# Performance work log

Measured on AMD Instinct MI355X. Metric: run time of the kernel, lower is better.

## Reference

```python
import jax, jax.numpy as jnp
import numpy as np

THRESH = 0.5     # confidence threshold (forward arg 'thresh' in the original)
IOU_THR = 0.1    # nms(boxes, 0.1) in the original
K = 512          # fixed top-k candidates per scale (static-shape stand-in for nonzero())


def _decode(output, anchors, stride, k):
    """Filter + parse for one scale. output: [B, 3*(5+nc), H, W]."""
    B, C, H, W = output.shape
    o = output.transpose(0, 2, 3, 1).reshape(B, H, W, 3, -1)   # [B,H,W,3,5+nc]
    D = o.shape[-1]
    conf = jax.nn.sigmoid(o[..., 0]).reshape(-1)               # [B*H*W*3]
    scores, idx = jax.lax.top_k(conf, k)                       # fixed-size filter
    n, h, w, a = jnp.unravel_index(idx, (B, H, W, 3))
    v = o.reshape(-1, D)[idx]                                  # [K, 5+nc]
    dt = v.dtype
    cy = (h.astype(dt) + jax.nn.sigmoid(v[:, 2])) * stride
    cx = (w.astype(dt) + jax.nn.sigmoid(v[:, 1])) * stride
    bw = anchors[a, 0] * jnp.exp(v[:, 3])
    bh = anchors[a, 1] * jnp.exp(v[:, 4])
    cond = jax.nn.sigmoid(v[:, 0])
    cls = jnp.argmax(v[:, 5:], axis=1).astype(dt)              # argmax(softmax)=argmax
    boxes = jnp.stack([n.astype(dt), cond, cx, cy, bw, bh, cls], axis=1)  # [K,7]
    valid = cond > THRESH
    return boxes, valid


def _nms(boxes, valid, iou_thr):
    """Greedy per-image, per-class NMS. boxes: [N,7] = (n, cond, cx, cy, w, h, cls)."""
    N = boxes.shape[0]
    score = jnp.where(valid, boxes[:, 1], -jnp.inf)
    order = jnp.argsort(-score)
    b = boxes[order]
    val = valid[order]
    x1 = b[:, 2] - b[:, 4] * 0.5
    y1 = b[:, 3] - b[:, 5] * 0.5
    x2 = b[:, 2] + b[:, 4] * 0.5
    y2 = b[:, 3] + b[:, 5] * 0.5
    area = b[:, 4] * b[:, 5]
    ix1 = jnp.maximum(x1[:, None], x1[None, :])
    iy1 = jnp.maximum(y1[:, None], y1[None, :])
    ix2 = jnp.minimum(x2[:, None], x2[None, :])
    iy2 = jnp.minimum(y2[:, None], y2[None, :])
    inter = jnp.clip(ix2 - ix1, 0) * jnp.clip(iy2 - iy1, 0)
    iou = inter / (area[:, None] + area[None, :] - inter + 1e-9)
    same = (b[:, 0, None] == b[None, :, 0]) & (b[:, 6, None] == b[None, :, 6])
    overlap = (iou > iou_thr) & same                           # [N,N] bool, no grad needed
    rng = jnp.arange(N)

    def body(i, supp):
        row = overlap[i] & (rng > i)
        active = (~supp[i]) & val[i]
        return jnp.where(active, supp | row, supp)

    supp = jax.lax.fori_loop(0, N, body, jnp.zeros(N, bool))
    keep = val & (~supp)
    return b * keep[:, None].astype(b.dtype), keep


def setup_inputs() -> dict:
    key = jax.random.key(0)
    ks = jax.random.split(key, 6)
    B, C = 64, 255  # 3 * (5 + 80 classes)
    return {
        "output_13": jax.random.normal(ks[0], (B, C, 13, 13), jnp.float32),
        "output_26": jax.random.normal(ks[1], (B, C, 26, 26), jnp.float32),
        "output_52": jax.random.normal(ks[2], (B, C, 52, 52), jnp.float32),
        "anchors_13": jax.random.uniform(ks[3], (3, 2), jnp.float32, 90.0, 330.0),
        "anchors_26": jax.random.uniform(ks[4], (3, 2), jnp.float32, 30.0, 120.0),
        "anchors_52": jax.random.uniform(ks[5], (3, 2), jnp.float32, 10.0, 60.0),
    }


def reference(output_13, output_26, output_52, anchors_13, anchors_26, anchors_52):
    b13, v13 = _decode(output_13, anchors_13, 32.0, K)
    b26, v26 = _decode(output_26, anchors_26, 16.0, K)
    b52, v52 = _decode(output_52, anchors_52, 8.0, K)
    boxes = jnp.concatenate([b13, b26, b52], axis=0)   # [3K, 7]
    valid = jnp.concatenate([v13, v26, v52], axis=0)
    final_boxes, keep = _nms(boxes, valid, IOU_THR)
    return final_boxes, keep
```

## Files before the change

### kernel.cpp

```cpp
#include <hip/hip_runtime.h>
#include <stdint.h>

#define K_SEL 512
#define NBOX 1536
#define CAND_CAP 4096
#define HBITS 13
#define HBINS 8192
#define NSHARD 128
#define SEG 128
#define HBLK 64
#define HB0 8
#define HB1 16
#define HB2 40
#define ICAP 56

#define M0 32448
#define M1 129792
#define M2 519168
#define M_TOT (M0+M1+M2)

#define OFF_HIST 0u
#define OFF_CNT  98304u
#define OFF_THR  99840u
#define OFF_CAND 99872u
#define OFF_BOX  493088u
#define OFF_SKEY 536096u
#define OFF_TOPK 548384u
#define ZERO_BYTES 99840u

typedef unsigned long long u64;
typedef uint32_t u32;
typedef uint16_t u16;

__device__ __forceinline__ float sigf(float x) { return 1.0f / (1.0f + expf(-x)); }

__device__ __forceinline__ u32 fmono(float f) {
    u32 u = __float_as_uint(f);
    return (u & 0x80000000u) ? ~u : (u | 0x80000000u);
}

__global__ __launch_bounds__(1024) void k_hist(const float* p0, const float* p1, const float* p2,
                                               uint8_t* ws) {
    __shared__ u32 lh[HBINS];
    for (int i = threadIdx.x; i < HBINS; i += 1024) lh[i] = 0;
    __syncthreads();
    int b = blockIdx.x, s, b0, nb;
    if (b < HB0)            { s = 0; b0 = b;             nb = HB0; }
    else if (b < HB0 + HB1) { s = 1; b0 = b - HB0;       nb = HB1; }
    else                    { s = 2; b0 = b - HB0 - HB1; nb = HB2; }
    int M = (s == 0) ? M0 : (s == 1) ? M1 : M2;
    int H = (s == 0) ? 13 : (s == 1) ? 26 : 52;
    int HW = H * H;
    const float* p = (s == 0) ? p0 : (s == 1) ? p1 : p2;
    for (int o = b0 * 1024 + threadIdx.x; o < M; o += nb * 1024) {
        int n = o / (3 * HW); int rem = o - n * 3 * HW;
        int a = rem / HW;     int pix = rem - a * HW;
        float conf = sigf(p[(size_t)(n * 255 + a * 85) * HW + pix]);
        atomicAdd(&lh[fmono(conf) >> (32 - HBITS)], 1u);
    }
    __syncthreads();
    u32* gh = (u32*)(ws + OFF_HIST) + s * HBINS;
    for (int i = threadIdx.x; i < HBINS; i += 1024) {
        u32 v = lh[i];
        if (v) atomicAdd(&gh[i], v);
    }
}

__global__ __launch_bounds__(1024) void k_scan(uint8_t* ws) {
    int s = blockIdx.x;
    u32* hist = (u32*)(ws + OFF_HIST) + s * HBINS;
    __shared__ u32 sum[1024];
    int t = threadIdx.x;
    u32 bins[8];
    const uint4* hp = (const uint4*)(hist + t * 8);
    uint4 x = hp[0], y = hp[1];
    bins[0] = x.x; bins[1] = x.y; bins[2] = x.z; bins[3] = x.w;
    bins[4] = y.x; bins[5] = y.y; bins[6] = y.z; bins[7] = y.w;
    u32 acc = 0;
#pragma unroll
    for (int k = 0; k < 8; ++k) acc += bins[k];
    sum[t] = acc;
    __syncthreads();
    for (int off = 1; off < 1024; off <<= 1) {
        u32 v = (t + off < 1024) ? sum[t + off] : 0;
        __syncthreads();
        sum[t] += v;
        __syncthreads();
    }
    u32 excl = (t < 1023) ? sum[t + 1] : 0;
    u32 mine = sum[t] - excl;
    if (excl < K_SEL && excl + mine >= K_SEL) {
        u32 cum = excl; int thr = t * 8;
#pragma unroll
        for (int k = 7; k >= 0; --k) {
            cum += bins[k];
            if (cum >= K_SEL) { thr = t * 8 + k; break; }
        }
        ((u32*)(ws + OFF_THR))[s] = (u32)thr;
    }
}

__global__ __launch_bounds__(1024) void k_compact(const float* p0, const float* p1, const float* p2,
                                                  uint8_t* ws) {
    int t = blockIdx.x * 1024 + threadIdx.x;
    if (t >= M_TOT) return;
    int s, o, H;
    if (t < M0)            { s = 0; o = t;           H = 13; }
    else if (t < M0 + M1)  { s = 1; o = t - M0;      H = 26; }
    else                   { s = 2; o = t - M0 - M1; H = 52; }
    const float* p = (s == 0) ? p0 : (s == 1) ? p1 : p2;
    int HW = H * H;
    int n = o / (3 * HW); int rem = o - n * 3 * HW;
    int a = rem / HW;     int pix = rem - a * HW;
    float conf = sigf(p[(size_t)(n * 255 + a * 85) * HW + pix]);
    u32 cb = fmono(conf);
    if ((cb >> (32 - HBITS)) >= ((u32*)(ws + OFF_THR))[s]) {
        int c = n * (3 * HW) + pix * 3 + a;
        int idx = s * NSHARD + (blockIdx.x & (NSHARD - 1));
        u32 pos = atomicAdd(&((u32*)(ws + OFF_CNT))[idx], 1u);
        if (pos < SEG) {
            u64 key = ((u64)cb << 32) | (u32)(~(u32)c);
            ((u64*)(ws + OFF_CAND))[(u32)idx * SEG + pos] = key;
        }
    }
}

__global__ __launch_bounds__(1024) void k_sortsel(uint8_t* ws) {
    int s = blockIdx.x;
    __shared__ u64 a_[CAND_CAP];
    __shared__ u32 scnt[NSHARD], spre[NSHARD];
    __shared__ u32 total_s;
    int t = threadIdx.x;
    if (t < NSHARD) {
        u32 v = ((u32*)(ws + OFF_CNT))[s * NSHARD + t];
        scnt[t] = (v > SEG) ? SEG : v;
        spre[t] = scnt[t];
    }
    __syncthreads();
    for (int off = 1; off < NSHARD; off <<= 1) {
        u32 v = (t >= off && t < NSHARD) ? spre[t - off] : 0;
        __syncthreads();
        if (t < NSHARD) spre[t] += v;
        __syncthreads();
    }
    if (t == 0) total_s = (spre[NSHARD - 1] > CAND_CAP) ? CAND_CAP : spre[NSHARD - 1];
    __syncthreads();
    u32 total = total_s;
    int n2 = K_SEL;
    while (n2 < (int)total) n2 <<= 1;
    for (int i = t; i < n2; i += 1024) a_[i] = 0ull;
    __syncthreads();
    if (t < NSHARD) {
        u32 base = spre[t] - scnt[t];
        const u64* seg = (const u64*)(ws + OFF_CAND) + (u32)(s * NSHARD + t) * SEG;
        for (u32 i = 0; i < scnt[t]; ++i)
            if (base + i < CAND_CAP) a_[base + i] = seg[i];
    }
    __syncthreads();
    for (int k = 2; k <= n2; k <<= 1) {
        for (int j = k >> 1; j > 0; j >>= 1) {
            for (int i = t; i < n2; i += 1024) {
                int ixj = i ^ j;
                if (ixj > i) {
                    bool desc = ((i & k) == 0);
                    u64 x = a_[i], y = a_[ixj];
                    if (desc ? (x < y) : (x > y)) { a_[i] = y; a_[ixj] = x; }
                }
            }
            __syncthreads();
        }
    }
    u64* topk = (u64*)(ws + OFF_TOPK) + s * K_SEL;
    for (int r = t; r < K_SEL; r += 1024) topk[r] = a_[r];
}

__global__ __launch_bounds__(1024) void k_decode(const float* p0, const float* p1, const float* p2,
                                                 const float* a0, const float* a1, const float* a2,
                                                 uint8_t* ws) {
    int t = blockIdx.x * 1024 + threadIdx.x;
    int g = t >> 4, l = t & 15;
    if (g >= NBOX) return;
    int s = g >> 9, r = g & 511;
    int H = (s == 0) ? 13 : (s == 1) ? 26 : 52;
    float stride = (s == 0) ? 32.f : (s == 1) ? 16.f : 8.f;
    const float* p    = (s == 0) ? p0 : (s == 1) ? p1 : p2;
    const float* anch = (s == 0) ? a0 : (s == 1) ? a1 : a2;
    int HW = H * H, hw3 = HW * 3;
    u64 key = ((u64*)(ws + OFF_TOPK))[g];
    int c = (int)(~(u32)key);
    int n = c / hw3; int rem = c - n * hw3;
    int pix = rem / 3; int aa = rem - pix * 3;
    size_t base = (size_t)(n * 255 + aa * 85) * HW + pix;
    float best = -INFINITY; int bi = 0x7FFFFFFF;
#pragma unroll
    for (int m = 0; m < 5; ++m) {
        int k2 = l + m * 16;
        float vv = p[base + (size_t)(5 + k2) * HW];
        if (vv > best) { best = vv; bi = k2; }
    }
    float vload = (l < 5) ? p[base + (size_t)l * HW] : 0.f;
#pragma unroll
    for (int off = 8; off > 0; off >>= 1) {
        float ov = __shfl_down(best, off, 16);
        int oi = __shfl_down(bi, off, 16);
        if (ov > best || (ov == best && oi < bi)) { best = ov; bi = oi; }
    }
    float v0 = __shfl(vload, 0, 16);
    float v1 = __shfl(vload, 1, 16);
    float v2 = __shfl(vload, 2, 16);
    float v3 = __shfl(vload, 3, 16);
    float v4 = __shfl(vload, 4, 16);
    if (l == 0) {
        int h = pix / H, w = pix - h * H;
        float conf = sigf(v0);
        float cx = ((float)w + sigf(v1)) * stride;
        float cy = ((float)h + sigf(v2)) * stride;
        float bw = anch[aa * 2 + 0] * expf(v3);
        float bh = anch[aa * 2 + 1] * expf(v4);
        float* box = (float*)(ws + OFF_BOX) + g * 7;
        box[0] = (float)n; box[1] = conf; box[2] = cx; box[3] = cy;
        box[4] = bw; box[5] = bh; box[6] = (float)bi;
        u32 mono = (conf > 0.5f) ? fmono(conf) : fmono(-INFINITY);
        ((u64*)(ws + OFF_SKEY))[g] = ((u64)mono << 32) | (u32)(~(u32)g);
    }
}

__global__ __launch_bounds__(1024) void k_tail(uint8_t* ws, float* out) {
    __shared__ u64 sk[NBOX];
    __shared__ u16 srt[NBOX];
    __shared__ float gx1[NBOX], gy1[NBOX], gx2[NBOX], gy2[NBOX], gar[NBOX];
    __shared__ u32 meta[NBOX];
    __shared__ uint8_t gkeep[NBOX];
    __shared__ u16 lists[64 * ICAP];
    __shared__ u32 icnt[64];
    u32* wvcnt = (u32*)sk;
    int t = threadIdx.x;
    u64* skey = (u64*)(ws + OFF_SKEY);
    for (int i = t; i < NBOX; i += 1024) sk[i] = skey[i];
    __syncthreads();
    for (int i = t; i < NBOX; i += 1024) {
        int s = i >> 9, r = i & 511;
        u64 K = sk[i];
        int g = r;
#pragma unroll
        for (int s2 = 0; s2 < 3; ++s2) {
            if (s2 == s) continue;
            const u64* seg = &sk[s2 << 9];
            int lo = 0, hi = 512;
            while (lo < hi) {
                int mid = (lo + hi) >> 1;
                if (seg[mid] > K) lo = mid + 1; else hi = mid;
            }
            g += lo;
        }
        srt[g] = (u16)i;
    }
    __syncthreads();
    const float* box = (const float*)(ws + OFF_BOX);
    for (int i = t; i < NBOX; i += 1024) {
        int pos = srt[i];
        float b0 = box[pos * 7 + 0], b1 = box[pos * 7 + 1], b2 = box[pos * 7 + 2];
        float b3 = box[pos * 7 + 3], b4 = box[pos * 7 + 4], b5 = box[pos * 7 + 5];
        float b6 = box[pos * 7 + 6];
        gx1[i] = b2 - b4 * 0.5f;  gy1[i] = b3 - b5 * 0.5f;
        gx2[i] = b2 + b4 * 0.5f;  gy2[i] = b3 + b5 * 0.5f;
        gar[i] = b4 * b5;
        meta[i] = (u32)(int)b0 | ((u32)(int)b6 << 8) | ((b1 > 0.5f) ? (1u << 16) : 0u);
        gkeep[i] = 0;
        wvcnt[i] = 0;
    }
    __syncthreads();
#pragma unroll
    for (int pass = 0; pass < 2; ++pass) {
        int ii = t + pass * 1024;
        u32 img = (ii < NBOX) ? (meta[ii] & 63u) : 0u;
        u64 mask = ~0ull;
#pragma unroll
        for (int b = 0; b < 6; ++b) {
            bool bit = (img >> b) & 1u;
            u64 bal = __ballot(bit);
            mask &= bit ? bal : ~bal;
        }
        if (ii < NBOX) {
            int lane = ii & 63;
            int wrank = __popcll(mask & ((1ull << lane) - 1ull));
            if (wrank == 0) wvcnt[(ii >> 6) * 64 + img] = (u32)__popcll(mask);
        }
    }
    __syncthreads();
    if (t < 64) {
        u32 c = 0;
        for (int w = 0; w < 24; ++w) c += wvcnt[w * 64 + t];
        icnt[t] = c;
    }
#pragma unroll
    for (int pass = 0; pass < 2; ++pass) {
        int ii = t + pass * 1024;
        u32 img = (ii < NBOX) ? (meta[ii] & 63u) : 0u;
        u64 mask = ~0ull;
#pragma unroll
        for (int b = 0; b < 6; ++b) {
            bool bit = (img >> b) & 1u;
            u64 bal = __ballot(bit);
            mask &= bit ? bal : ~bal;
        }
        if (ii < NBOX) {
            int lane = ii & 63;
            int wv = ii >> 6;
            int r = __popcll(mask & ((1ull << lane) - 1ull));
            for (int w = 0; w < wv; ++w) r += (int)wvcnt[w * 64 + img];
            if (r < ICAP) lists[img * ICAP + r] = (u16)ii;
        }
    }
    __syncthreads();
    {
        int wv = t >> 6, lane = t & 63;
        for (int im = wv * 4; im < wv * 4 + 4; ++im) {
            int cnt = (int)icnt[im]; if (cnt > ICAP) cnt = ICAP;
            float x1 = 0, y1 = 0, x2 = 0, y2 = 0, ar = 0;
            u32 cl = 0; int u = -1; bool val = false;
            if (lane < cnt) {
                u = lists[im * ICAP + lane];
                x1 = gx1[u]; y1 = gy1[u]; x2 = gx2[u]; y2 = gy2[u]; ar = gar[u];
                u32 m = meta[u]; cl = (m >> 8) & 0xFFu; val = (m >> 16) & 1u;
            }
            u64 valmask = __ballot(val);
            u64 keptmask = 0;
            for (int a = 0; a < cnt; ++a) {
                float ax1 = __shfl(x1, a), ay1 = __shfl(y1, a);
                float ax2 = __shfl(x2, a), ay2 = __shfl(y2, a);
                float aar = __shfl(ar, a);
                u32 acl = (u32)__shfl((int)cl, a);
                float ix1 = fmaxf(x1, ax1), iy1 = fmaxf(y1, ay1);
                float ix2 = fminf(x2, ax2), iy2 = fminf(y2, ay2);
                float iw = fmaxf(ix2 - ix1, 0.f), ih = fmaxf(iy2 - iy1, 0.f);
                float inter = iw * ih;
                float iou = inter / (ar + aar - inter + 1e-9f);
                bool viol = (lane < a) && ((keptmask >> lane) & 1ull) &&
                            (cl == acl) && (iou > 0.1f);
                u64 bal = __ballot(viol);
                bool kept = ((valmask >> a) & 1ull) && (bal == 0ull);
                if (kept) keptmask |= (1ull << a);
            }
            if (lane < cnt) gkeep[u] = (uint8_t)((keptmask >> lane) & 1ull);
        }
    }
    __syncthreads();
    for (int i = t; i < NBOX; i += 1024) {
        float kf = gkeep[i] ? 1.f : 0.f;
        int pos = srt[i];
        for (int k = 0; k < 7; ++k) out[i * 7 + k] = box[pos * 7 + k] * kf;
        out[NBOX * 7 + i] = kf;
    }
}

extern "C" void kernel_launch(void* const* d_in, const int* in_sizes, int n_in,
                              void* d_out, int out_size, void* d_ws, size_t ws_size,
                              hipStream_t stream) {
    const float* p0 = (const float*)d_in[0];
    const float* p1 = (const float*)d_in[1];
    const float* p2 = (const float*)d_in[2];
    const float* a0 = (const float*)d_in[3];
    const float* a1 = (const float*)d_in[4];
    const float* a2 = (const float*)d_in[5];
    uint8_t* ws = (uint8_t*)d_ws;
    float* out = (float*)d_out;

    const int CB = (M_TOT + 1023) / 1024;

    hipMemsetAsync(ws, 0, ZERO_BYTES, stream);
    k_hist   <<<HBLK, 1024, 0, stream>>>(p0, p1, p2, ws);
    k_scan   <<<3, 1024, 0, stream>>>(ws);
    k_compact<<<CB, 1024, 0, stream>>>(p0, p1, p2, ws);
    k_sortsel<<<3, 1024, 0, stream>>>(ws);
    k_decode <<<24, 1024, 0, stream>>>(p0, p1, p2, a0, a1, a2, ws);
    k_tail   <<<1, 1024, 0, stream>>>(ws, out);
}
```

Measured before the change: 118.0 us.

## Fuse scan into compact and sort into decode, drop memset

The histogram kernel now writes per-block histogram slices and zeroes the shard counters itself, so the memset and its global atomics go away. Each compact block re-reduces its scale's slices and scans them to find the threshold locally, removing the separate scan launch. The per-scale sort is replicated across 64 blocks per scale, and each block decodes 8 of the top-k entries straight from shared memory, removing the sort and decode split. This cuts the launch count from six to four at the cost of redundant histogram reduction and sorting, and fewer histogram and compact blocks.

```diff
diff --git a/kernel.cpp b/kernel.cpp
--- a/kernel.cpp
+++ b/kernel.cpp
@@ -3,15 +3,11 @@
 
 #define K_SEL 512
 #define NBOX 1536
-#define CAND_CAP 4096
 #define HBITS 13
 #define HBINS 8192
 #define NSHARD 128
 #define SEG 128
-#define HBLK 64
-#define HB0 8
-#define HB1 16
-#define HB2 40
+#define HBLK 24
 #define ICAP 56
 
 #define M0 32448
@@ -19,14 +15,11 @@
 #define M2 519168
 #define M_TOT (M0+M1+M2)
 
-#define OFF_HIST 0u
-#define OFF_CNT  98304u
-#define OFF_THR  99840u
-#define OFF_CAND 99872u
-#define OFF_BOX  493088u
-#define OFF_SKEY 536096u
-#define OFF_TOPK 548384u
-#define ZERO_BYTES 99840u
+#define OFF_HSL  0u
+#define OFF_CNT  786432u
+#define OFF_CAND 787968u
+#define OFF_BOX  1181184u
+#define OFF_SKEY 1224192u
 
 typedef unsigned long long u64;
 typedef uint32_t u32;
@@ -42,40 +35,49 @@
 __global__ __launch_bounds__(1024) void k_hist(const float* p0, const float* p1, const float* p2,
                                                uint8_t* ws) {
     __shared__ u32 lh[HBINS];
-    for (int i = threadIdx.x; i < HBINS; i += 1024) lh[i] = 0;
+    int t = threadIdx.x;
+    for (int i = t; i < HBINS; i += 1024) lh[i] = 0;
+    if (blockIdx.x == 0 && t < 3 * NSHARD) ((u32*)(ws + OFF_CNT))[t] = 0;
     __syncthreads();
     int b = blockIdx.x, s, b0, nb;
-    if (b < HB0)            { s = 0; b0 = b;             nb = HB0; }
-    else if (b < HB0 + HB1) { s = 1; b0 = b - HB0;       nb = HB1; }
-    else                    { s = 2; b0 = b - HB0 - HB1; nb = HB2; }
+    if (b < 2)      { s = 0; b0 = b;     nb = 2;  }
+    else if (b < 8) { s = 1; b0 = b - 2; nb = 6;  }
+    else            { s = 2; b0 = b - 8; nb = 16; }
     int M = (s == 0) ? M0 : (s == 1) ? M1 : M2;
     int H = (s == 0) ? 13 : (s == 1) ? 26 : 52;
     int HW = H * H;
     const float* p = (s == 0) ? p0 : (s == 1) ? p1 : p2;
-    for (int o = b0 * 1024 + threadIdx.x; o < M; o += nb * 1024) {
+    for (int o = b0 * 1024 + t; o < M; o += nb * 1024) {
         int n = o / (3 * HW); int rem = o - n * 3 * HW;
         int a = rem / HW;     int pix = rem - a * HW;
         float conf = sigf(p[(size_t)(n * 255 + a * 85) * HW + pix]);
         atomicAdd(&lh[fmono(conf) >> (32 - HBITS)], 1u);
     }
     __syncthreads();
-    u32* gh = (u32*)(ws + OFF_HIST) + s * HBINS;
-    for (int i = threadIdx.x; i < HBINS; i += 1024) {
-        u32 v = lh[i];
-        if (v) atomicAdd(&gh[i], v);
-    }
-}
-
-__global__ __launch_bounds__(1024) void k_scan(uint8_t* ws) {
-    int s = blockIdx.x;
-    u32* hist = (u32*)(ws + OFF_HIST) + s * HBINS;
+    u32* slice = (u32*)(ws + OFF_HSL) + (u32)b * HBINS;
+    for (int i = t; i < HBINS; i += 1024) slice[i] = lh[i];
+}
+
+__global__ __launch_bounds__(1024) void k_compact(const float* p0, const float* p1, const float* p2,
+                                                  uint8_t* ws) {
     __shared__ u32 sum[1024];
-    int t = threadIdx.x;
+    __shared__ u32 thr_sh;
+    int bid = blockIdx.x, t = threadIdx.x;
+    int s, lb, nb;
+    if (bid < 12)      { s = 0; lb = bid;      nb = 12;  }
+    else if (bid < 60) { s = 1; lb = bid - 12; nb = 48;  }
+    else               { s = 2; lb = bid - 60; nb = 196; }
+    int sb0 = (s == 0) ? 0 : (s == 1) ? 2 : 8;
+    int sb1 = (s == 0) ? 2 : (s == 1) ? 8 : 24;
     u32 bins[8];
-    const uint4* hp = (const uint4*)(hist + t * 8);
-    uint4 x = hp[0], y = hp[1];
-    bins[0] = x.x; bins[1] = x.y; bins[2] = x.z; bins[3] = x.w;
-    bins[4] = y.x; bins[5] = y.y; bins[6] = y.z; bins[7] = y.w;
+#pragma unroll
+    for (int k = 0; k < 8; ++k) bins[k] = 0;
+    for (int b = sb0; b < sb1; ++b) {
+        const uint4* sl = (const uint4*)((u32*)(ws + OFF_HSL) + (u32)b * HBINS + t * 8);
+        uint4 x = sl[0], y = sl[1];
+        bins[0] += x.x; bins[1] += x.y; bins[2] += x.z; bins[3] += x.w;
+        bins[4] += y.x; bins[5] += y.y; bins[6] += y.z; bins[7] += y.w;
+    }
     u32 acc = 0;
 #pragma unroll
     for (int k = 0; k < 8; ++k) acc += bins[k];
@@ -96,40 +98,37 @@
             cum += bins[k];
             if (cum >= K_SEL) { thr = t * 8 + k; break; }
         }
-        ((u32*)(ws + OFF_THR))[s] = (u32)thr;
-    }
-}
-
-__global__ __launch_bounds__(1024) void k_compact(const float* p0, const float* p1, const float* p2,
+        thr_sh = (u32)thr;
+    }
+    __syncthreads();
+    u32 thr = thr_sh;
+    int M = (s == 0) ? M0 : (s == 1) ? M1 : M2;
+    int H = (s == 0) ? 13 : (s == 1) ? 26 : 52;
+    int HW = H * H;
+    const float* p = (s == 0) ? p0 : (s == 1) ? p1 : p2;
+    for (int o = lb * 1024 + t; o < M; o += nb * 1024) {
+        int n = o / (3 * HW); int rem = o - n * 3 * HW;
+        int a = rem / HW;     int pix = rem - a * HW;
+        float conf = sigf(p[(size_t)(n * 255 + a * 85) * HW + pix]);
+        u32 cb = fmono(conf);
+        if ((cb >> (32 - HBITS)) >= thr) {
+            int c = n * (3 * HW) + pix * 3 + a;
+            int idx = s * NSHARD + (bid & (NSHARD - 1));
+            u32 pos = atomicAdd(&((u32*)(ws + OFF_CNT))[idx], 1u);
+            if (pos < SEG) {
+                u64 key = ((u64)cb << 32) | (u32)(~(u32)c);
+                ((u64*)(ws + OFF_CAND))[(u32)idx * SEG + pos] = key;
+            }
+        }
+    }
+}
+
+__global__ __launch_bounds__(1024) void k_sortdec(const float* p0, const float* p1, const float* p2,
+                                                  const float* a0, const float* a1, const float* a2,
                                                   uint8_t* ws) {
-    int t = blockIdx.x * 1024 + threadIdx.x;
-    if (t >= M_TOT) return;
-    int s, o, H;
-    if (t < M0)            { s = 0; o = t;           H = 13; }
-    else if (t < M0 + M1)  { s = 1; o = t - M0;      H = 26; }
-    else                   { s = 2; o = t - M0 - M1; H = 52; }
-    const float* p = (s == 0) ? p0 : (s == 1) ? p1 : p2;
-    int HW = H * H;
-    int n = o / (3 * HW); int rem = o - n * 3 * HW;
-    int a = rem / HW;     int pix = rem - a * HW;
-    float conf = sigf(p[(size_t)(n * 255 + a * 85) * HW + pix]);
-    u32 cb = fmono(conf);
-    if ((cb >> (32 - HBITS)) >= ((u32*)(ws + OFF_THR))[s]) {
-        int c = n * (3 * HW) + pix * 3 + a;
-        int idx = s * NSHARD + (blockIdx.x & (NSHARD - 1));
-        u32 pos = atomicAdd(&((u32*)(ws + OFF_CNT))[idx], 1u);
-        if (pos < SEG) {
-            u64 key = ((u64)cb << 32) | (u32)(~(u32)c);
-            ((u64*)(ws + OFF_CAND))[(u32)idx * SEG + pos] = key;
-        }
-    }
-}
-
-__global__ __launch_bounds__(1024) void k_sortsel(uint8_t* ws) {
-    int s = blockIdx.x;
-    __shared__ u64 a_[CAND_CAP];
+    int s = blockIdx.x >> 6, sub = blockIdx.x & 63;
+    __shared__ u64 a_[4096];
     __shared__ u32 scnt[NSHARD], spre[NSHARD];
-    __shared__ u32 total_s;
     int t = threadIdx.x;
     if (t < NSHARD) {
         u32 v = ((u32*)(ws + OFF_CNT))[s * NSHARD + t];
@@ -143,9 +142,8 @@
         if (t < NSHARD) spre[t] += v;
         __syncthreads();
     }
-    if (t == 0) total_s = (spre[NSHARD - 1] > CAND_CAP) ? CAND_CAP : spre[NSHARD - 1];
-    __syncthreads();
-    u32 total = total_s;
+    u32 total = spre[NSHARD - 1];
+    if (total > 4096) total = 4096;
     int n2 = K_SEL;
     while (n2 < (int)total) n2 <<= 1;
     for (int i = t; i < n2; i += 1024) a_[i] = 0ull;
@@ -154,7 +152,7 @@
         u32 base = spre[t] - scnt[t];
         const u64* seg = (const u64*)(ws + OFF_CAND) + (u32)(s * NSHARD + t) * SEG;
         for (u32 i = 0; i < scnt[t]; ++i)
-            if (base + i < CAND_CAP) a_[base + i] = seg[i];
+            if (base + i < 4096) a_[base + i] = seg[i];
     }
     __syncthreads();
     for (int k = 2; k <= n2; k <<= 1) {
@@ -170,23 +168,15 @@
             __syncthreads();
         }
     }
-    u64* topk = (u64*)(ws + OFF_TOPK) + s * K_SEL;
-    for (int r = t; r < K_SEL; r += 1024) topk[r] = a_[r];
-}
-
-__global__ __launch_bounds__(1024) void k_decode(const float* p0, const float* p1, const float* p2,
-                                                 const float* a0, const float* a1, const float* a2,
-                                                 uint8_t* ws) {
-    int t = blockIdx.x * 1024 + threadIdx.x;
-    int g = t >> 4, l = t & 15;
-    if (g >= NBOX) return;
-    int s = g >> 9, r = g & 511;
+    if (t >= 128) return;
+    int g16 = t >> 4, l = t & 15;
+    int rloc = sub * 8 + g16;
     int H = (s == 0) ? 13 : (s == 1) ? 26 : 52;
     float stride = (s == 0) ? 32.f : (s == 1) ? 16.f : 8.f;
     const float* p    = (s == 0) ? p0 : (s == 1) ? p1 : p2;
     const float* anch = (s == 0) ? a0 : (s == 1) ? a1 : a2;
     int HW = H * H, hw3 = HW * 3;
-    u64 key = ((u64*)(ws + OFF_TOPK))[g];
+    u64 key = a_[rloc];
     int c = (int)(~(u32)key);
     int n = c / hw3; int rem = c - n * hw3;
     int pix = rem / 3; int aa = rem - pix * 3;
@@ -217,11 +207,12 @@
         float cy = ((float)h + sigf(v2)) * stride;
         float bw = anch[aa * 2 + 0] * expf(v3);
         float bh = anch[aa * 2 + 1] * expf(v4);
-        float* box = (float*)(ws + OFF_BOX) + g * 7;
+        int gi = s * K_SEL + rloc;
+        float* box = (float*)(ws + OFF_BOX) + gi * 7;
         box[0] = (float)n; box[1] = conf; box[2] = cx; box[3] = cy;
         box[4] = bw; box[5] = bh; box[6] = (float)bi;
         u32 mono = (conf > 0.5f) ? fmono(conf) : fmono(-INFINITY);
-        ((u64*)(ws + OFF_SKEY))[g] = ((u64)mono << 32) | (u32)(~(u32)g);
+        ((u64*)(ws + OFF_SKEY))[gi] = ((u64)mono << 32) | (u32)(~(u32)gi);
     }
 }
 
@@ -306,9 +297,9 @@
         }
         if (ii < NBOX) {
             int lane = ii & 63;
-            int wv = ii >> 6;
+            int wvv = ii >> 6;
             int r = __popcll(mask & ((1ull << lane) - 1ull));
-            for (int w = 0; w < wv; ++w) r += (int)wvcnt[w * 64 + img];
+            for (int w = 0; w < wvv; ++w) r += (int)wvcnt[w * 64 + img];
             if (r < ICAP) lists[img * ICAP + r] = (u16)ii;
         }
     }
@@ -366,13 +357,8 @@
     uint8_t* ws = (uint8_t*)d_ws;
     float* out = (float*)d_out;
 
-    const int CB = (M_TOT + 1023) / 1024;
-
-    hipMemsetAsync(ws, 0, ZERO_BYTES, stream);
     k_hist   <<<HBLK, 1024, 0, stream>>>(p0, p1, p2, ws);
-    k_scan   <<<3, 1024, 0, stream>>>(ws);
-    k_compact<<<CB, 1024, 0, stream>>>(p0, p1, p2, ws);
-    k_sortsel<<<3, 1024, 0, stream>>>(ws);
-    k_decode <<<24, 1024, 0, stream>>>(p0, p1, p2, a0, a1, a2, ws);
+    k_compact<<<256, 1024, 0, stream>>>(p0, p1, p2, ws);
+    k_sortdec<<<192, 1024, 0, stream>>>(p0, p1, p2, a0, a1, a2, ws);
     k_tail   <<<1, 1024, 0, stream>>>(ws, out);
 }
```

Measured after the change: 125.4 us. +6.3%, slower.

## Replace global histogram atomics with per-block slices and drop memset launch

Applied to the files above, without the earlier changes.

Each histogram block now writes its own 8192-bin slice to workspace instead of atomically adding into a shared global histogram, and the scan kernel sums the slices for its scale. The shared-memory histogram is split into two copies, chosen by wave parity, to reduce LDS atomic contention. The block count rises from 64 to 96, with more blocks given to the larger scales. The separate hipMemsetAsync is removed, with block 0 of the histogram kernel zeroing the shard counters, which drops one launch at the cost of more workspace traffic and a longer scan loop.

```diff
diff --git a/kernel.cpp b/kernel.cpp
--- a/kernel.cpp
+++ b/kernel.cpp
@@ -3,15 +3,11 @@
 
 #define K_SEL 512
 #define NBOX 1536
-#define CAND_CAP 4096
 #define HBITS 13
 #define HBINS 8192
 #define NSHARD 128
 #define SEG 128
-#define HBLK 64
-#define HB0 8
-#define HB1 16
-#define HB2 40
+#define HBLK 96
 #define ICAP 56
 
 #define M0 32448
@@ -19,14 +15,13 @@
 #define M2 519168
 #define M_TOT (M0+M1+M2)
 
-#define OFF_HIST 0u
-#define OFF_CNT  98304u
-#define OFF_THR  99840u
-#define OFF_CAND 99872u
-#define OFF_BOX  493088u
-#define OFF_SKEY 536096u
-#define OFF_TOPK 548384u
-#define ZERO_BYTES 99840u
+#define OFF_HSL  0u
+#define OFF_CNT  3145728u
+#define OFF_THR  3147264u
+#define OFF_CAND 3147296u
+#define OFF_BOX  3540512u
+#define OFF_SKEY 3583520u
+#define OFF_TOPK 3595808u
 
 typedef unsigned long long u64;
 typedef uint32_t u32;
@@ -41,41 +36,46 @@
 
 __global__ __launch_bounds__(1024) void k_hist(const float* p0, const float* p1, const float* p2,
                                                uint8_t* ws) {
-    __shared__ u32 lh[HBINS];
-    for (int i = threadIdx.x; i < HBINS; i += 1024) lh[i] = 0;
+    __shared__ u32 lh[2 * HBINS];
+    int t = threadIdx.x;
+    for (int i = t; i < 2 * HBINS; i += 1024) lh[i] = 0;
+    if (blockIdx.x == 0 && t < 3 * NSHARD) ((u32*)(ws + OFF_CNT))[t] = 0;
     __syncthreads();
     int b = blockIdx.x, s, b0, nb;
-    if (b < HB0)            { s = 0; b0 = b;             nb = HB0; }
-    else if (b < HB0 + HB1) { s = 1; b0 = b - HB0;       nb = HB1; }
-    else                    { s = 2; b0 = b - HB0 - HB1; nb = HB2; }
+    if (b < 8)       { s = 0; b0 = b;      nb = 8;  }
+    else if (b < 32) { s = 1; b0 = b - 8;  nb = 24; }
+    else             { s = 2; b0 = b - 32; nb = 64; }
     int M = (s == 0) ? M0 : (s == 1) ? M1 : M2;
     int H = (s == 0) ? 13 : (s == 1) ? 26 : 52;
     int HW = H * H;
     const float* p = (s == 0) ? p0 : (s == 1) ? p1 : p2;
-    for (int o = b0 * 1024 + threadIdx.x; o < M; o += nb * 1024) {
+    u32 cofs = ((u32)(t >> 6) & 1u) * HBINS;
+    for (int o = b0 * 1024 + t; o < M; o += nb * 1024) {
         int n = o / (3 * HW); int rem = o - n * 3 * HW;
         int a = rem / HW;     int pix = rem - a * HW;
         float conf = sigf(p[(size_t)(n * 255 + a * 85) * HW + pix]);
-        atomicAdd(&lh[fmono(conf) >> (32 - HBITS)], 1u);
-    }
-    __syncthreads();
-    u32* gh = (u32*)(ws + OFF_HIST) + s * HBINS;
-    for (int i = threadIdx.x; i < HBINS; i += 1024) {
-        u32 v = lh[i];
-        if (v) atomicAdd(&gh[i], v);
-    }
+        atomicAdd(&lh[cofs + (fmono(conf) >> (32 - HBITS))], 1u);
+    }
+    __syncthreads();
+    u32* slice = (u32*)(ws + OFF_HSL) + (u32)b * HBINS;
+    for (int i = t; i < HBINS; i += 1024) slice[i] = lh[i] + lh[HBINS + i];
 }
 
 __global__ __launch_bounds__(1024) void k_scan(uint8_t* ws) {
     int s = blockIdx.x;
-    u32* hist = (u32*)(ws + OFF_HIST) + s * HBINS;
+    int b0 = (s == 0) ? 0 : (s == 1) ? 8 : 32;
+    int b1 = (s == 0) ? 8 : (s == 1) ? 32 : 96;
     __shared__ u32 sum[1024];
     int t = threadIdx.x;
     u32 bins[8];
-    const uint4* hp = (const uint4*)(hist + t * 8);
-    uint4 x = hp[0], y = hp[1];
-    bins[0] = x.x; bins[1] = x.y; bins[2] = x.z; bins[3] = x.w;
-    bins[4] = y.x; bins[5] = y.y; bins[6] = y.z; bins[7] = y.w;
+#pragma unroll
+    for (int k = 0; k < 8; ++k) bins[k] = 0;
+    for (int b = b0; b < b1; ++b) {
+        const uint4* sl = (const uint4*)((u32*)(ws + OFF_HSL) + (u32)b * HBINS + t * 8);
+        uint4 x = sl[0], y = sl[1];
+        bins[0] += x.x; bins[1] += x.y; bins[2] += x.z; bins[3] += x.w;
+        bins[4] += y.x; bins[5] += y.y; bins[6] += y.z; bins[7] += y.w;
+    }
     u32 acc = 0;
 #pragma unroll
     for (int k = 0; k < 8; ++k) acc += bins[k];
@@ -127,9 +127,8 @@
 
 __global__ __launch_bounds__(1024) void k_sortsel(uint8_t* ws) {
     int s = blockIdx.x;
-    __shared__ u64 a_[CAND_CAP];
+    __shared__ u64 a_[4096];
     __shared__ u32 scnt[NSHARD], spre[NSHARD];
-    __shared__ u32 total_s;
     int t = threadIdx.x;
     if (t < NSHARD) {
         u32 v = ((u32*)(ws + OFF_CNT))[s * NSHARD + t];
@@ -143,9 +142,8 @@
         if (t < NSHARD) spre[t] += v;
         __syncthreads();
     }
-    if (t == 0) total_s = (spre[NSHARD - 1] > CAND_CAP) ? CAND_CAP : spre[NSHARD - 1];
-    __syncthreads();
-    u32 total = total_s;
+    u32 total = spre[NSHARD - 1];
+    if (total > 4096) total = 4096;
     int n2 = K_SEL;
     while (n2 < (int)total) n2 <<= 1;
     for (int i = t; i < n2; i += 1024) a_[i] = 0ull;
@@ -154,7 +152,7 @@
         u32 base = spre[t] - scnt[t];
         const u64* seg = (const u64*)(ws + OFF_CAND) + (u32)(s * NSHARD + t) * SEG;
         for (u32 i = 0; i < scnt[t]; ++i)
-            if (base + i < CAND_CAP) a_[base + i] = seg[i];
+            if (base + i < 4096) a_[base + i] = seg[i];
     }
     __syncthreads();
     for (int k = 2; k <= n2; k <<= 1) {
@@ -180,7 +178,7 @@
     int t = blockIdx.x * 1024 + threadIdx.x;
     int g = t >> 4, l = t & 15;
     if (g >= NBOX) return;
-    int s = g >> 9, r = g & 511;
+    int s = g >> 9;
     int H = (s == 0) ? 13 : (s == 1) ? 26 : 52;
     float stride = (s == 0) ? 32.f : (s == 1) ? 16.f : 8.f;
     const float* p    = (s == 0) ? p0 : (s == 1) ? p1 : p2;
@@ -306,9 +304,9 @@
         }
         if (ii < NBOX) {
             int lane = ii & 63;
-            int wv = ii >> 6;
+            int wvv = ii >> 6;
             int r = __popcll(mask & ((1ull << lane) - 1ull));
-            for (int w = 0; w < wv; ++w) r += (int)wvcnt[w * 64 + img];
+            for (int w = 0; w < wvv; ++w) r += (int)wvcnt[w * 64 + img];
             if (r < ICAP) lists[img * ICAP + r] = (u16)ii;
         }
     }
@@ -368,7 +366,6 @@
 
     const int CB = (M_TOT + 1023) / 1024;
 
-    hipMemsetAsync(ws, 0, ZERO_BYTES, stream);
     k_hist   <<<HBLK, 1024, 0, stream>>>(p0, p1, p2, ws);
     k_scan   <<<3, 1024, 0, stream>>>(ws);
     k_compact<<<CB, 1024, 0, stream>>>(p0, p1, p2, ws);
```

Result: slower. 134.0 us (+13.6%).
